# Optimization experiments

Measured on AMD Instinct MI355X. Metric: run time of the kernel, lower is better.

The kernel has to match this reference:

```python
import jax, jax.numpy as jnp
import numpy as np

EPS = 1e-5

def silu(x):
    return x * jax.nn.sigmoid(x)

def layernorm(x, g, b):
    m = jnp.mean(x, axis=-1, keepdims=True)
    v = jnp.var(x, axis=-1, keepdims=True)
    return (x - m) * jax.lax.rsqrt(v + EPS) * g + b

def mamba(x, in_w, conv_w, conv_b, xproj_w, dt_w, dt_b, A_log, Dp, out_w):
    # x: (B, L, d_model)
    B_, L, _ = x.shape
    d_inner, d_conv = conv_w.shape
    d_state = A_log.shape[1]
    dt_rank = dt_w.shape[1]
    xz = x @ in_w.T                     # (B, L, 2*d_inner)
    u, z = jnp.split(xz, 2, axis=-1)
    # causal depthwise conv1d, kernel size d_conv, truncated to L
    up = jnp.pad(u, ((0, 0), (d_conv - 1, 0), (0, 0))).transpose(0, 2, 1)  # (B, C, L+K-1)
    uc = jax.lax.conv_general_dilated(up, conv_w[:, None, :], (1,), 'VALID',
                                      feature_group_count=d_inner)        # (B, C, L)
    u = silu(uc.transpose(0, 2, 1) + conv_b)                               # (B, L, d_inner)
    dbc = u @ xproj_w.T                                                    # (B, L, dt_rank+2*d_state)
    dt, Bm, Cm = jnp.split(dbc, [dt_rank, dt_rank + d_state], axis=-1)
    delta = jax.nn.softplus(dt @ dt_w.T + dt_b)                            # (B, L, d_inner)
    A = -jnp.exp(A_log)                                                    # (d_inner, d_state)
    dA = jnp.exp(delta[..., None] * A)                                     # (B, L, d_inner, d_state)
    dBu = delta[..., None] * Bm[:, :, None, :] * u[..., None]

    def step(h, inp):
        dA_t, dBu_t, C_t = inp
        h = dA_t * h + dBu_t                                               # (B, d_inner, d_state)
        y = jnp.einsum('bdn,bn->bd', h, C_t)
        return h, y

    h0 = jnp.zeros((B_, d_inner, d_state), x.dtype)
    _, ys = jax.lax.scan(step, h0, (dA.transpose(1, 0, 2, 3),
                                    dBu.transpose(1, 0, 2, 3),
                                    Cm.transpose(1, 0, 2)))
    y = ys.transpose(1, 0, 2) + u * Dp
    y = y * silu(z)
    return y @ out_w.T

def decoder_layer(x,
                  f_in_w, f_conv_w, f_conv_b, f_xproj_w, f_dt_w, f_dt_b, f_A_log, f_D, f_out_w,
                  r_in_w, r_conv_w, r_conv_b, r_xproj_w, r_dt_w, r_dt_b, r_A_log, r_D, r_out_w,
                  conv1_w, conv1_b, conv2_w, conv2_b, ln1_g, ln1_b, ln2_g, ln2_b):
    fwd = mamba(x, f_in_w, f_conv_w, f_conv_b, f_xproj_w, f_dt_w, f_dt_b, f_A_log, f_D, f_out_w)
    bwd = jnp.flip(mamba(jnp.flip(x, axis=1), r_in_w, r_conv_w, r_conv_b, r_xproj_w,
                         r_dt_w, r_dt_b, r_A_log, r_D, r_out_w), axis=1)
    x1 = layernorm(x + fwd + bwd, ln1_g, ln1_b)
    # kernel-size-1 Conv1d == pointwise linear; dropout is identity at eval
    y = jax.nn.gelu(x1 @ conv1_w.T + conv1_b, approximate=False)
    y = y @ conv2_w.T + conv2_b
    return layernorm(x1 + y, ln2_g, ln2_b)

def setup_inputs() -> dict:
    key = jax.random.key(0)
    ks = jax.random.split(key, 32)
    d_model, d_state, d_inner, dt_rank, d_ff = 512, 16, 1024, 32, 2048
    B, L = 8, 512
    s = 0.02
    inp = {}
    inp['x'] = jax.random.normal(ks[0], (B, L, d_model), jnp.float32)
    i = 1
    for p in ('f', 'r'):
        inp[p + '_in_w'] = jax.random.normal(ks[i], (2 * d_inner, d_model)) * s; i += 1
        inp[p + '_conv_w'] = jax.random.normal(ks[i], (d_inner, 4)) * 0.2; i += 1
        inp[p + '_conv_b'] = jax.random.normal(ks[i], (d_inner,)) * s; i += 1
        inp[p + '_xproj_w'] = jax.random.normal(ks[i], (dt_rank + 2 * d_state, d_inner)) * s; i += 1
        inp[p + '_dt_w'] = jax.random.normal(ks[i], (d_inner, dt_rank)) * s; i += 1
        inp[p + '_dt_b'] = jax.random.normal(ks[i], (d_inner,)) * s; i += 1
        inp[p + '_A_log'] = jax.random.uniform(ks[i], (d_inner, d_state)); i += 1
        inp[p + '_D'] = jax.random.normal(ks[i], (d_inner,)) * s + 1.0; i += 1
        inp[p + '_out_w'] = jax.random.normal(ks[i], (d_model, d_inner)) * s; i += 1
    inp['conv1_w'] = jax.random.normal(ks[i], (d_ff, d_model)) * s; i += 1
    inp['conv1_b'] = jax.random.normal(ks[i], (d_ff,)) * s; i += 1
    inp['conv2_w'] = jax.random.normal(ks[i], (d_model, d_ff)) * s; i += 1
    inp['conv2_b'] = jax.random.normal(ks[i], (d_model,)) * s; i += 1
    inp['ln1_g'] = jnp.ones((d_model,)); inp['ln1_b'] = jnp.zeros((d_model,))
    inp['ln2_g'] = jnp.ones((d_model,)); inp['ln2_b'] = jnp.zeros((d_model,))
    return inp

def reference(x,
              f_in_w, f_conv_w, f_conv_b, f_xproj_w, f_dt_w, f_dt_b, f_A_log, f_D, f_out_w,
              r_in_w, r_conv_w, r_conv_b, r_xproj_w, r_dt_w, r_dt_b, r_A_log, r_D, r_out_w,
              conv1_w, conv1_b, conv2_w, conv2_b, ln1_g, ln1_b, ln2_g, ln2_b):
    return decoder_layer(x,
                         f_in_w, f_conv_w, f_conv_b, f_xproj_w, f_dt_w, f_dt_b, f_A_log, f_D, f_out_w,
                         r_in_w, r_conv_w, r_conv_b, r_xproj_w, r_dt_w, r_dt_b, r_A_log, r_D, r_out_w,
                         conv1_w, conv1_b, conv2_w, conv2_b, ln1_g, ln1_b, ln2_g, ln2_b)
```

## Files before the change

kernel.cpp:

```cpp
#include <hip/hip_runtime.h>
#include <hip/hip_bf16.h>

#define DEVINL __device__ __forceinline__

typedef short bf16x8 __attribute__((ext_vector_type(8)));
typedef float f32x4 __attribute__((ext_vector_type(4)));
typedef ushort ushort8v __attribute__((ext_vector_type(8)));

static constexpr int Bn = 8, Ln = 512, DM = 512, DI = 1024, DS = 16, DFF = 2048;
static constexpr int Mtok = Bn * Ln;
static constexpr int NCH = 32, CLS = 16;

DEVINL float bf2f(ushort u) { union { uint i; float f; } v; v.i = uint(u) << 16; return v.f; }
DEVINL ushort f2bf(float f) {
  union { float f; uint i; } v; v.f = f;
  uint r = v.i + 0x7FFF + ((v.i >> 16) & 1);
  return ushort(r >> 16);
}

#if __has_builtin(__builtin_amdgcn_exp2f)
#define EXP2F(x) __builtin_amdgcn_exp2f(x)
#else
#define EXP2F(x) __expf((x) * 0.69314718056f)
#endif

#define GLOAD16(gp, lp)                                                        \
  __builtin_amdgcn_global_load_lds(                                            \
      (const __attribute__((address_space(1))) void*)(gp),                     \
      (__attribute__((address_space(3))) void*)(lp), 16, 0, 0)

struct CvtJob { const float* src; ushort* dst; int blk0; int _pad; };
struct CvtTab { CvtJob j[11]; };

__global__ __launch_bounds__(256)
void cvt_k(CvtTab tb, int njobs) {
  const int blk = blockIdx.x;
  int ji = 0;
#pragma unroll
  for (int k = 1; k < 11; ++k)
    if (k < njobs && tb.j[k].blk0 <= blk) ji = k;
  const CvtJob J = tb.j[ji];
  const size_t base = (size_t)(blk - J.blk0) * 2048 + (size_t)threadIdx.x * 8;
  float4 a = *(const float4*)(J.src + base);
  float4 b = *(const float4*)(J.src + base + 4);
  ushort8v o;
  o[0] = f2bf(a.x); o[1] = f2bf(a.y); o[2] = f2bf(a.z); o[3] = f2bf(a.w);
  o[4] = f2bf(b.x); o[5] = f2bf(b.y); o[6] = f2bf(b.z); o[7] = f2bf(b.w);
  *(ushort8v*)(J.dst + base) = o;
}

template<int BM, int BN, int WM, int WN, int EPI, int OUTF32, int DUALK>
__global__ __launch_bounds__(256)
void gemm_lds(const ushort* __restrict__ A0, const ushort* __restrict__ W0,
              void* __restrict__ C0v, const float* __restrict__ bias0,
              const ushort* __restrict__ A1, const ushort* __restrict__ W1,
              void* __restrict__ C1v, const float* __restrict__ bias1,
              const ushort* __restrict__ Ab0, const ushort* __restrict__ Wb0,
              int K, int lda, int ldw, int ldc, int Kb, int ldab, int ldwb)
{
  constexpr int MT = BM / WM / 16, NT = BN / WN / 16;
  constexpr int RA = BM * 32 / 2048, RB = BN * 32 / 2048;
  __shared__ ushort As[BM * 32];
  __shared__ ushort Bs[BN * 32];

  const ushort* Ap = blockIdx.z ? A1 : A0;
  const ushort* Wp = blockIdx.z ? W1 : W0;
  void* Cv         = blockIdx.z ? C1v : C0v;
  const float* bia = blockIdx.z ? bias1 : bias0;

  const int tid = threadIdx.x, lane = tid & 63, wv = tid >> 6;
  const int wm = wv / WN, wn = wv % WN;
  const int mbase = blockIdx.x * BM, nbase = blockIdx.y * BN;
  const int r = lane & 15, ko = (lane >> 4) * 8;

  f32x4 acc[MT][NT];
#pragma unroll
  for (int mi = 0; mi < MT; ++mi)
#pragma unroll
    for (int ni = 0; ni < NT; ++ni) acc[mi][ni] = (f32x4){0.f, 0.f, 0.f, 0.f};

  for (int blkK = 0; blkK < (DUALK ? 2 : 1); ++blkK) {
    const ushort* Au = (DUALK && blkK) ? Ab0 : Ap;
    const ushort* Wu = (DUALK && blkK) ? Wb0 : Wp;
    const int Ku  = (DUALK && blkK) ? Kb : K;
    const int ldau = (DUALK && blkK) ? ldab : lda;
    const int ldwu = (DUALK && blkK) ? ldwb : ldw;

    for (int k0 = 0; k0 < Ku; k0 += 32) {
      __syncthreads();
#pragma unroll
      for (int i = 0; i < RA; ++i) {
        const int e = i * 2048 + wv * 512 + lane * 8;
        const int row = e >> 5, ck = e & 31;
        GLOAD16(Au + (size_t)(mbase + row) * ldau + k0 + ck,
                (ushort*)As + i * 2048 + wv * 512);
      }
#pragma unroll
      for (int i = 0; i < RB; ++i) {
        const int e = i * 2048 + wv * 512 + lane * 8;
        const int row = e >> 5, ck = e & 31;
        GLOAD16(Wu + (size_t)(nbase + row) * ldwu + k0 + ck,
                (ushort*)Bs + i * 2048 + wv * 512);
      }
      __syncthreads();

      bf16x8 af[MT], bfv[NT];
#pragma unroll
      for (int mi = 0; mi < MT; ++mi)
        af[mi] = *(const bf16x8*)&As[(wm * MT * 16 + mi * 16 + r) * 32 + ko];
#pragma unroll
      for (int ni = 0; ni < NT; ++ni)
        bfv[ni] = *(const bf16x8*)&Bs[(wn * NT * 16 + ni * 16 + r) * 32 + ko];
#pragma unroll
      for (int mi = 0; mi < MT; ++mi)
#pragma unroll
        for (int ni = 0; ni < NT; ++ni)
          acc[mi][ni] = __builtin_amdgcn_mfma_f32_16x16x32_bf16(af[mi], bfv[ni], acc[mi][ni], 0, 0, 0);
    }
  }

  const int rr = (lane >> 4) * 4, cc = lane & 15;
#pragma unroll
  for (int ni = 0; ni < NT; ++ni) {
    const int col = nbase + wn * NT * 16 + ni * 16 + cc;
    float bsv = 0.f;
    if (EPI >= 1) bsv = bia[col];
#pragma unroll
    for (int mi = 0; mi < MT; ++mi) {
#pragma unroll
      for (int j = 0; j < 4; ++j) {
        const int row = mbase + wm * MT * 16 + mi * 16 + rr + j;
        float v = acc[mi][ni][j] + bsv;
        if (EPI == 2) v = (v > 20.f) ? v : __logf(1.f + __expf(v));
        if (EPI == 3) v = 0.5f * v * (1.f + erff(v * 0.70710678f));
        if (OUTF32) ((float*)Cv)[(size_t)row * ldc + col] = v;
        else        ((ushort*)Cv)[(size_t)row * ldc + col] = f2bf(v);
      }
    }
  }
}

template<int WAVES_M, int WAVES_N, int MT, int NT, int EPI, int OUTF32, int BLKOUT>
__global__ __launch_bounds__(WAVES_M * WAVES_N * 64)
void gemm_k(const ushort* __restrict__ A0, const ushort* __restrict__ W0,
            void* __restrict__ C0v, const float* __restrict__ bias0,
            const ushort* __restrict__ A1, const ushort* __restrict__ W1,
            void* __restrict__ C1v, const float* __restrict__ bias1,
            int K, int lda, int ldw, int ldc)
{
  const ushort* A   = blockIdx.z ? A1 : A0;
  const ushort* W   = blockIdx.z ? W1 : W0;
  void* Cv          = blockIdx.z ? C1v : C0v;
  const float* bia  = blockIdx.z ? bias1 : bias0;

  const int tid = threadIdx.x, lane = tid & 63, wv = tid >> 6;
  const int wm = wv / WAVES_N, wn = wv % WAVES_N;
  const int r = lane & 15, ko = (lane >> 4) * 8;
  const int mbase = blockIdx.x * (WAVES_M * MT * 16) + wm * (MT * 16);
  const int nbase = blockIdx.y * (WAVES_N * NT * 16) + wn * (NT * 16);

  f32x4 acc[MT][NT];
#pragma unroll
  for (int mi = 0; mi < MT; ++mi)
#pragma unroll
    for (int ni = 0; ni < NT; ++ni) acc[mi][ni] = (f32x4){0.f, 0.f, 0.f, 0.f};

  const ushort* arow[MT];
  const ushort* wrow[NT];
#pragma unroll
  for (int mi = 0; mi < MT; ++mi) arow[mi] = A + (size_t)(mbase + mi * 16 + r) * lda + ko;
#pragma unroll
  for (int ni = 0; ni < NT; ++ni) wrow[ni] = W + (size_t)(nbase + ni * 16 + r) * ldw + ko;
  for (int k0 = 0; k0 < K; k0 += 32) {
    bf16x8 av[MT], bv[NT];
#pragma unroll
    for (int mi = 0; mi < MT; ++mi) av[mi] = *(const bf16x8*)(arow[mi] + k0);
#pragma unroll
    for (int ni = 0; ni < NT; ++ni) bv[ni] = *(const bf16x8*)(wrow[ni] + k0);
#pragma unroll
    for (int mi = 0; mi < MT; ++mi)
#pragma unroll
      for (int ni = 0; ni < NT; ++ni)
        acc[mi][ni] = __builtin_amdgcn_mfma_f32_16x16x32_bf16(av[mi], bv[ni], acc[mi][ni], 0, 0, 0);
  }

  const int rr = (lane >> 4) * 4, cc = lane & 15;
  if constexpr (BLKOUT) {
    __shared__ ushort tile[64][65];
#pragma unroll
    for (int ni = 0; ni < NT; ++ni) {
      const int col = nbase + ni * 16 + cc;
      float bsv = (EPI >= 1) ? bia[col] : 0.f;
#pragma unroll
      for (int mi = 0; mi < MT; ++mi) {
#pragma unroll
        for (int j = 0; j < 4; ++j) {
          float v = acc[mi][ni][j] + bsv;
          if (EPI == 2) v = (v > 20.f) ? v : __logf(1.f + __expf(v));
          const int rl = (wm * MT + mi) * 16 + rr + j;
          const int cl = (wn * NT + ni) * 16 + cc;
          tile[rl][cl] = f2bf(v);
        }
      }
    }
    __syncthreads();
    const int rc = tid >> 6, coll = tid & 63;
    const int mblk = blockIdx.x * (WAVES_M * MT * 16);
    const int nblk = blockIdx.y * (WAVES_N * NT * 16);
    ushort8v o0, o1;
#pragma unroll
    for (int jj = 0; jj < 8; ++jj) {
      o0[jj] = tile[rc * 16 + jj][coll];
      o1[jj] = tile[rc * 16 + 8 + jj][coll];
    }
    const size_t base = ((size_t)((mblk >> 4) + rc) * ldc + nblk + coll) * 16;
    *(ushort8v*)((ushort*)Cv + base) = o0;
    *(ushort8v*)((ushort*)Cv + base + 8) = o1;
  } else {
#pragma unroll
    for (int ni = 0; ni < NT; ++ni) {
      const int col = nbase + ni * 16 + cc;
      float bsv = 0.f;
      if (EPI >= 1) bsv = bia[col];
#pragma unroll
      for (int mi = 0; mi < MT; ++mi) {
#pragma unroll
        for (int j = 0; j < 4; ++j) {
          const int row = mbase + mi * 16 + rr + j;
          float v = acc[mi][ni][j] + bsv;
          if (EPI == 2) v = (v > 20.f) ? v : __logf(1.f + __expf(v));
          if (OUTF32) ((float*)Cv)[(size_t)row * ldc + col] = v;
          else        ((ushort*)Cv)[(size_t)row * ldc + col] = f2bf(v);
        }
      }
    }
  }
}

__global__ __launch_bounds__(256)
void xproj_k(const ushort* __restrict__ A0, const ushort* __restrict__ W0,
             ushort* __restrict__ C0,
             const ushort* __restrict__ A1, const ushort* __restrict__ W1,
             ushort* __restrict__ C1)
{
  const ushort* A = blockIdx.z ? A1 : A0;
  const ushort* W = blockIdx.z ? W1 : W0;
  ushort* C       = blockIdx.z ? C1 : C0;

  const int tid = threadIdx.x, lane = tid & 63, wv = tid >> 6;
  const int r = lane & 15, ko = (lane >> 4) * 8;
  const int mbase = blockIdx.x * 16;
  const int nbase = wv * 16;

  f32x4 acc = (f32x4){0.f, 0.f, 0.f, 0.f};
  const ushort* ap = A + (size_t)(mbase + r) * DI + ko;
  const ushort* wp = W + (size_t)(nbase + r) * DI + ko;
#pragma unroll 4
  for (int k0 = 0; k0 < DI; k0 += 32) {
    const bf16x8 av = *(const bf16x8*)(ap + k0);
    const bf16x8 bv = *(const bf16x8*)(wp + k0);
    acc = __builtin_amdgcn_mfma_f32_16x16x32_bf16(av, bv, acc, 0, 0, 0);
  }
  const int cc = lane & 15, rr = (lane >> 4) * 4;
#pragma unroll
  for (int j = 0; j < 4; ++j)
    C[(size_t)(mbase + rr + j) * 64 + nbase + cc] = f2bf(acc[j]);
}

#define CONV_LOADW(pos, dst)                                                   \
  if ((pos) >= 0 && (pos) < Ln) {                                              \
    const ushort4 xv = *(const ushort4*)(xz + (size_t)(bLn + (pos)) * 2048 + c0); \
    dst[0] = bf2f(xv.x); dst[1] = bf2f(xv.y);                                  \
    dst[2] = bf2f(xv.z); dst[3] = bf2f(xv.w);                                  \
  } else { dst[0] = 0.f; dst[1] = 0.f; dst[2] = 0.f; dst[3] = 0.f; }

#define CONV_STEP(tpos, s)                                                     \
  {                                                                            \
    _Pragma("unroll")                                                          \
    for (int ch = 0; ch < 4; ++ch) {                                           \
      wa[ch] = wb[ch]; wb[ch] = wc[ch]; wc[ch] = wd[ch];                       \
    }                                                                          \
    {                                                                          \
      const ushort4 xv = *(const ushort4*)(xz + (size_t)(bLn + (tpos)) * 2048 + c0); \
      wd[0] = bf2f(xv.x); wd[1] = bf2f(xv.y);                                  \
      wd[2] = bf2f(xv.z); wd[3] = bf2f(xv.w);                                  \
    }                                                                          \
    const ushort4 zv = *(const ushort4*)(xz + (size_t)(bLn + (tpos)) * 2048 + DI + c0); \
    float zf[4];                                                               \
    zf[0] = bf2f(zv.x); zf[1] = bf2f(zv.y); zf[2] = bf2f(zv.z); zf[3] = bf2f(zv.w); \
    ushort4 ur;                                                                \
    _Pragma("unroll")                                                          \
    for (int ch = 0; ch < 4; ++ch) {                                           \
      float sa = bias[ch] + wgt[ch][0] * wa[ch] + wgt[ch][1] * wb[ch]          \
               + wgt[ch][2] * wc[ch] + wgt[ch][3] * wd[ch];                    \
      const ushort su = f2bf(sa / (1.f + __expf(-sa)));                        \
      ubuf[ch][(s) >> 3][(s) & 7] = su;                                        \
      ((ushort*)&ur)[ch] = su;                                                 \
      gbuf[ch][(s) >> 3][(s) & 7] = f2bf(zf[ch] / (1.f + __expf(-zf[ch])));    \
    }                                                                          \
    *(ushort4*)(uo + (size_t)(bLn + (tpos)) * 1024 + c0) = ur;                 \
  }

__global__ __launch_bounds__(256, 2)
void conv_k(const ushort* __restrict__ xz_f, const ushort* __restrict__ xz_r,
            const float* __restrict__ fw, const float* __restrict__ fb,
            const float* __restrict__ rw, const float* __restrict__ rb,
            ushort* __restrict__ u_f, ushort* __restrict__ u_r,
            ushort* __restrict__ ub_f, ushort* __restrict__ ub_r,
            ushort* __restrict__ gb_f, ushort* __restrict__ gb_r)
{
  const int idx = blockIdx.x * 256 + threadIdx.x;
  const int cg = idx & 255, chunk = (idx >> 8) & 31, b = (idx >> 13) & 7, dir = idx >> 16;
  const int c0 = cg * 4;
  const int bLn = b * Ln;

  const ushort* xz = dir ? xz_r : xz_f;
  const float* cw = dir ? rw : fw;
  const float* cb = dir ? rb : fb;
  ushort* uo = dir ? u_r : u_f;
  ushort* ub = dir ? ub_r : ub_f;
  ushort* gb = dir ? gb_r : gb_f;

  float bias[4];
  float wgt[4][4];
#pragma unroll
  for (int ch = 0; ch < 4; ++ch) {
    bias[ch] = cb[c0 + ch];
    const float4 w4 = *(const float4*)(cw + (size_t)(c0 + ch) * 4);
    wgt[ch][0] = w4.x; wgt[ch][1] = w4.y; wgt[ch][2] = w4.z; wgt[ch][3] = w4.w;
  }

  float wa[4], wb[4], wc[4], wd[4];
  ushort8v ubuf[4][2], gbuf[4][2];

  if (!dir) {
    const int t0 = chunk * 16;
    CONV_LOADW(t0 - 3, wb)
    CONV_LOADW(t0 - 2, wc)
    CONV_LOADW(t0 - 1, wd)
#pragma unroll
    for (int s = 0; s < 16; ++s) CONV_STEP(t0 + s, s)
  } else {
    const int t1 = chunk * 16 + 15;
    CONV_LOADW(t1 + 3, wb)
    CONV_LOADW(t1 + 2, wc)
    CONV_LOADW(t1 + 1, wd)
#pragma unroll
    for (int i = 0; i < 16; ++i) CONV_STEP(t1 - i, 15 - i)
  }

  const size_t blkBase = ((size_t)(b * 32 + chunk) * 1024 + c0) * 16;
#pragma unroll
  for (int ch = 0; ch < 4; ++ch) {
    *(ushort8v*)(ub + blkBase + (size_t)ch * 16)     = ubuf[ch][0];
    *(ushort8v*)(ub + blkBase + (size_t)ch * 16 + 8) = ubuf[ch][1];
    *(ushort8v*)(gb + blkBase + (size_t)ch * 16)     = gbuf[ch][0];
    *(ushort8v*)(gb + blkBase + (size_t)ch * 16 + 8) = gbuf[ch][1];
  }
}

#define SCAN1_STEP(s, e)                                                       \
  {                                                                            \
    const float dl = bf2f((ushort)(((e) < 8) ? dv0[(e)] : dv1[(e) - 8]));      \
    const float uv = bf2f((ushort)(((e) < 8) ? uv0[(e)] : uv1[(e) - 8]));      \
    const float du = dl * uv;                                                  \
    S += dl;                                                                   \
    _Pragma("unroll")                                                          \
    for (int g = 0; g < 4; ++g) {                                              \
      const float4 Bv = ((const float4*)Bs[(s)])[g];                           \
      h[g*4+0] = fmaf(EXP2F(dl * a2[g*4+0]), h[g*4+0], du * Bv.x);             \
      h[g*4+1] = fmaf(EXP2F(dl * a2[g*4+1]), h[g*4+1], du * Bv.y);             \
      h[g*4+2] = fmaf(EXP2F(dl * a2[g*4+2]), h[g*4+2], du * Bv.z);             \
      h[g*4+3] = fmaf(EXP2F(dl * a2[g*4+3]), h[g*4+3], du * Bv.w);             \
    }                                                                          \
  }

__global__ __launch_bounds__(256, 4)
void scan1_k(const ushort* __restrict__ db_f, const ushort* __restrict__ db_r,
             const ushort* __restrict__ ub_f, const ushort* __restrict__ ub_r,
             const ushort* __restrict__ dbc_f, const ushort* __restrict__ dbc_r,
             const float* __restrict__ fA, const float* __restrict__ rA,
             float4* __restrict__ hloc, float* __restrict__ Sa)
{
  const int bid = blockIdx.x;
  const int part = bid & 3, chunk = (bid >> 2) & 31, b = (bid >> 7) & 7, dir = bid >> 10;
  const int tid = threadIdx.x, c = part * 256 + tid;
  const int bd = dir * 8 + b;

  const ushort* dblk = dir ? db_r : db_f;
  const ushort* ublk = dir ? ub_r : ub_f;
  const ushort* dbc  = dir ? dbc_r : dbc_f;
  const float*  Alog = dir ? rA : fA;

  __shared__ float Bs[CLS][16];
  {
    const int s = tid >> 4, n = tid & 15;
    const int t = dir ? (Ln - 1 - (chunk * CLS + s)) : (chunk * CLS + s);
    Bs[s][n] = bf2f(dbc[(size_t)(b * Ln + t) * 64 + 32 + n]);
  }
  __syncthreads();

  float a2[16];
  {
    const float4* Ar = (const float4*)(Alog + (size_t)c * 16);
#pragma unroll
    for (int g = 0; g < 4; ++g) {
      float4 av = Ar[g];
      a2[g*4+0] = -__expf(av.x) * 1.44269504f;
      a2[g*4+1] = -__expf(av.y) * 1.44269504f;
      a2[g*4+2] = -__expf(av.z) * 1.44269504f;
      a2[g*4+3] = -__expf(av.w) * 1.44269504f;
    }
  }

  const int sc = dir ? (31 - chunk) : chunk;
  const size_t blkBase = (((size_t)(b * 32 + sc)) * 1024 + c) * 16;
  const ushort8v dv0 = *(const ushort8v*)(dblk + blkBase);
  const ushort8v dv1 = *(const ushort8v*)(dblk + blkBase + 8);
  const ushort8v uv0 = *(const ushort8v*)(ublk + blkBase);
  const ushort8v uv1 = *(const ushort8v*)(ublk + blkBase + 8);

  float h[16];
#pragma unroll
  for (int n = 0; n < 16; ++n) h[n] = 0.f;
  float S = 0.f;

  if (!dir) {
#pragma unroll
    for (int s = 0; s < CLS; ++s) SCAN1_STEP(s, s)
  } else {
#pragma unroll
    for (int s = 0; s < CLS; ++s) SCAN1_STEP(s, 15 - s)
  }

#pragma unroll
  for (int g = 0; g < 4; ++g) {
    const size_t o = ((size_t)g * 16 * NCH + (size_t)bd * NCH + chunk) * 1024 + c;
    hloc[o] = (float4){h[g*4+0], h[g*4+1], h[g*4+2], h[g*4+3]};
  }
  Sa[((size_t)bd * NCH + chunk) * 1024 + c] = S;
}

__global__ __launch_bounds__(256, 4)
void scan2_k(float4* __restrict__ hloc, const float* __restrict__ Sa,
             const float* __restrict__ fA, const float* __restrict__ rA)
{
  const int idx = blockIdx.x * 256 + threadIdx.x;
  const int ng = idx & 3, c = (idx >> 2) & 1023, b = (idx >> 12) & 7, dir = idx >> 15;
  const int bd = dir * 8 + b;
  const float* Alog = dir ? rA : fA;
  float a2[4];
  {
    const float4 av = *(const float4*)(Alog + (size_t)c * 16 + ng * 4);
    a2[0] = -__expf(av.x) * 1.44269504f;
    a2[1] = -__expf(av.y) * 1.44269504f;
    a2[2] = -__expf(av.z) * 1.44269504f;
    a2[3] = -__expf(av.w) * 1.44269504f;
  }
  float4 h = (float4){0.f, 0.f, 0.f, 0.f};
#pragma unroll
  for (int k = 0; k < NCH; ++k) {
    const size_t o = ((size_t)ng * 16 * NCH + (size_t)bd * NCH + k) * 1024 + c;
    const float S = Sa[((size_t)bd * NCH + k) * 1024 + c];
    const float4 hl = hloc[o];
    hloc[o] = h;
    h.x = fmaf(EXP2F(a2[0] * S), h.x, hl.x);
    h.y = fmaf(EXP2F(a2[1] * S), h.y, hl.y);
    h.z = fmaf(EXP2F(a2[2] * S), h.z, hl.z);
    h.w = fmaf(EXP2F(a2[3] * S), h.w, hl.w);
  }
}

#define SCAN3_STEP(s, e)                                                       \
  {                                                                            \
    const float dl = bf2f((ushort)(((e) < 8) ? dv0[(e)] : dv1[(e) - 8]));      \
    const float uv = bf2f((ushort)(((e) < 8) ? uv0[(e)] : uv1[(e) - 8]));      \
    const float gg = bf2f((ushort)(((e) < 8) ? gv0[(e)] : gv1[(e) - 8]));      \
    const float du = dl * uv;                                                  \
    float y = 0.f;                                                             \
    _Pragma("unroll")                                                          \
    for (int g = 0; g < 4; ++g) {                                              \
      const float4 Bv = ((const float4*)Bs[(s)])[g];                           \
      const float4 Cw = ((const float4*)Cs[(s)])[g];                           \
      h[g*4+0] = fmaf(EXP2F(dl * a2[g*4+0]), h[g*4+0], du * Bv.x);             \
      y = fmaf(h[g*4+0], Cw.x, y);                                             \
      h[g*4+1] = fmaf(EXP2F(dl * a2[g*4+1]), h[g*4+1], du * Bv.y);             \
      y = fmaf(h[g*4+1], Cw.y, y);                                             \
      h[g*4+2] = fmaf(EXP2F(dl * a2[g*4+2]), h[g*4+2], du * Bv.z);             \
      y = fmaf(h[g*4+2], Cw.z, y);                                             \
      h[g*4+3] = fmaf(EXP2F(dl * a2[g*4+3]), h[g*4+3], du * Bv.w);             \
      y = fmaf(h[g*4+3], Cw.w, y);                                             \
    }                                                                          \
    *ymp = f2bf((y + uv * Dc) * gg);                                           \
    ymp += stp;                                                                \
  }

__global__ __launch_bounds__(256, 4)
void scan3_k(const ushort* __restrict__ db_f, const ushort* __restrict__ db_r,
             const ushort* __restrict__ ub_f, const ushort* __restrict__ ub_r,
             const ushort* __restrict__ dbc_f, const ushort* __restrict__ dbc_r,
             const ushort* __restrict__ gb_f, const ushort* __restrict__ gb_r,
             const float* __restrict__ fA, const float* __restrict__ fD,
             const float* __restrict__ rA, const float* __restrict__ rD,
             const float4* __restrict__ hin,
             ushort* __restrict__ ym_f, ushort* __restrict__ ym_r)
{
  const int bid = blockIdx.x;
  const int part = bid & 3, chunk = (bid >> 2) & 31, b = (bid >> 7) & 7, dir = bid >> 10;
  const int tid = threadIdx.x, c = part * 256 + tid;
  const int bd = dir * 8 + b;

  const ushort* dblk = dir ? db_r : db_f;
  const ushort* ublk = dir ? ub_r : ub_f;
  const ushort* gblk = dir ? gb_r : gb_f;
  const ushort* dbc  = dir ? dbc_r : dbc_f;
  const float*  Alog = dir ? rA : fA;
  const float*  Dw   = dir ? rD : fD;
  ushort* ym         = dir ? ym_r : ym_f;

  __shared__ float Bs[CLS][16], Cs[CLS][16];
  {
    const int s = tid >> 5, k = tid & 31;
#pragma unroll
    for (int p = 0; p < 2; ++p) {
      const int ss = s + p * 8;
      const int t = dir ? (Ln - 1 - (chunk * CLS + ss)) : (chunk * CLS + ss);
      const float val = bf2f(dbc[(size_t)(b * Ln + t) * 64 + 32 + k]);
      if (k < 16) Bs[ss][k] = val; else Cs[ss][k - 16] = val;
    }
  }
  __syncthreads();

  float a2[16];
  {
    const float4* Ar = (const float4*)(Alog + (size_t)c * 16);
#pragma unroll
    for (int g = 0; g < 4; ++g) {
      float4 av = Ar[g];
      a2[g*4+0] = -__expf(av.x) * 1.44269504f;
      a2[g*4+1] = -__expf(av.y) * 1.44269504f;
      a2[g*4+2] = -__expf(av.z) * 1.44269504f;
      a2[g*4+3] = -__expf(av.w) * 1.44269504f;
    }
  }
  const float Dc = Dw[c];

  const int sc = dir ? (31 - chunk) : chunk;
  const size_t blkBase = (((size_t)(b * 32 + sc)) * 1024 + c) * 16;
  const ushort8v dv0 = *(const ushort8v*)(dblk + blkBase);
  const ushort8v dv1 = *(const ushort8v*)(dblk + blkBase + 8);
  const ushort8v uv0 = *(const ushort8v*)(ublk + blkBase);
  const ushort8v uv1 = *(const ushort8v*)(ublk + blkBase + 8);
  const ushort8v gv0 = *(const ushort8v*)(gblk + blkBase);
  const ushort8v gv1 = *(const ushort8v*)(gblk + blkBase + 8);

  float h[16];
#pragma unroll
  for (int g = 0; g < 4; ++g) {
    const size_t o = ((size_t)g * 16 * NCH + (size_t)bd * NCH + chunk) * 1024 + c;
    const float4 hv = hin[o];
    h[g*4+0] = hv.x; h[g*4+1] = hv.y; h[g*4+2] = hv.z; h[g*4+3] = hv.w;
  }

  const int t0 = dir ? (Ln - 1 - chunk * CLS) : (chunk * CLS);
  const int stp = (dir ? -1 : 1) * DI;
  ushort* ymp = ym + (size_t)(b * Ln + t0) * DI + c;

  if (!dir) {
#pragma unroll
    for (int s = 0; s < CLS; ++s) SCAN3_STEP(s, s)
  } else {
#pragma unroll
    for (int s = 0; s < CLS; ++s) SCAN3_STEP(s, 15 - s)
  }
}

template<int OUTF32>
__global__ __launch_bounds__(256)
void ln_k(const ushort* __restrict__ a, const ushort* __restrict__ b,
          const float* __restrict__ g, const float* __restrict__ bb,
          void* __restrict__ outv)
{
  const int row = blockIdx.x, tid = threadIdx.x;
  const size_t base = (size_t)row * DM;
  float v0 = bf2f(a[base + tid]) + bf2f(b[base + tid]);
  float v1 = bf2f(a[base + tid + 256]) + bf2f(b[base + tid + 256]);
  float s1 = v0 + v1, s2 = v0 * v0 + v1 * v1;
  for (int o = 32; o; o >>= 1) { s1 += __shfl_down(s1, o); s2 += __shfl_down(s2, o); }
  __shared__ float l1[4], l2[4];
  const int wv = tid >> 6, ln = tid & 63;
  if (ln == 0) { l1[wv] = s1; l2[wv] = s2; }
  __syncthreads();
  const float t1 = l1[0] + l1[1] + l1[2] + l1[3];
  const float t2 = l2[0] + l2[1] + l2[2] + l2[3];
  const float mean = t1 * (1.f / 512.f);
  const float var = t2 * (1.f / 512.f) - mean * mean;
  const float rs = rsqrtf(var + 1e-5f);
  const float o0 = (v0 - mean) * rs * g[tid] + bb[tid];
  const float o1 = (v1 - mean) * rs * g[tid + 256] + bb[tid + 256];
  if (OUTF32) {
    ((float*)outv)[base + tid] = o0;
    ((float*)outv)[base + tid + 256] = o1;
  } else {
    ((ushort*)outv)[base + tid] = f2bf(o0);
    ((ushort*)outv)[base + tid + 256] = f2bf(o1);
  }
}

extern "C" void kernel_launch(void* const* d_in, const int* in_sizes, int n_in,
                              void* d_out, int out_size, void* d_ws, size_t ws_size,
                              hipStream_t stream)
{
  const float* x        = (const float*)d_in[0];
  const float* f_in_w   = (const float*)d_in[1];
  const float* f_conv_w = (const float*)d_in[2];
  const float* f_conv_b = (const float*)d_in[3];
  const float* f_xproj  = (const float*)d_in[4];
  const float* f_dt_w   = (const float*)d_in[5];
  const float* f_dt_b   = (const float*)d_in[6];
  const float* f_A_log  = (const float*)d_in[7];
  const float* f_D      = (const float*)d_in[8];
  const float* f_out_w  = (const float*)d_in[9];
  const float* r_in_w   = (const float*)d_in[10];
  const float* r_conv_w = (const float*)d_in[11];
  const float* r_conv_b = (const float*)d_in[12];
  const float* r_xproj  = (const float*)d_in[13];
  const float* r_dt_w   = (const float*)d_in[14];
  const float* r_dt_b   = (const float*)d_in[15];
  const float* r_A_log  = (const float*)d_in[16];
  const float* r_D      = (const float*)d_in[17];
  const float* r_out_w  = (const float*)d_in[18];
  const float* conv1_w  = (const float*)d_in[19];
  const float* conv1_b  = (const float*)d_in[20];
  const float* conv2_w  = (const float*)d_in[21];
  const float* conv2_b  = (const float*)d_in[22];
  const float* ln1_g    = (const float*)d_in[23];
  const float* ln1_b    = (const float*)d_in[24];
  const float* ln2_g    = (const float*)d_in[25];
  const float* ln2_b    = (const float*)d_in[26];

  char* ws = (char*)d_ws;
  size_t off = 0;
  auto alloc = [&](size_t bytes) -> void* {
    void* p = ws + off;
    off += (bytes + 255) & ~(size_t)255;
    return p;
  };
  ushort* x_b     = (ushort*)alloc((size_t)Mtok * DM * 2);
  ushort* f_inw_b = (ushort*)alloc((size_t)2 * DI * DM * 2);
  ushort* r_inw_b = (ushort*)alloc((size_t)2 * DI * DM * 2);
  ushort* f_xp_b  = (ushort*)alloc((size_t)64 * DI * 2);
  ushort* r_xp_b  = (ushort*)alloc((size_t)64 * DI * 2);
  ushort* f_dtw_b = (ushort*)alloc((size_t)DI * 32 * 2);
  ushort* r_dtw_b = (ushort*)alloc((size_t)DI * 32 * 2);
  ushort* f_ow_b  = (ushort*)alloc((size_t)DM * DI * 2);
  ushort* r_ow_b  = (ushort*)alloc((size_t)DM * DI * 2);
  ushort* c1w_b   = (ushort*)alloc((size_t)DFF * DM * 2);
  ushort* c2w_b   = (ushort*)alloc((size_t)DM * DFF * 2);
  ushort* xz_f    = (ushort*)alloc((size_t)Mtok * 2048 * 2);
  ushort* xz_r    = (ushort*)alloc((size_t)Mtok * 2048 * 2);
  ushort* u_f     = (ushort*)alloc((size_t)Mtok * DI * 2);
  ushort* u_r     = (ushort*)alloc((size_t)Mtok * DI * 2);
  ushort* ub_f    = (ushort*)alloc((size_t)Mtok * DI * 2);
  ushort* ub_r    = (ushort*)alloc((size_t)Mtok * DI * 2);
  ushort* gb_f    = (ushort*)alloc((size_t)Mtok * DI * 2);
  ushort* gb_r    = (ushort*)alloc((size_t)Mtok * DI * 2);
  ushort* dbc_f   = (ushort*)alloc((size_t)Mtok * 64 * 2);
  ushort* dbc_r   = (ushort*)alloc((size_t)Mtok * 64 * 2);
  ushort* db_f    = (ushort*)alloc((size_t)Mtok * DI * 2);
  ushort* db_r    = (ushort*)alloc((size_t)Mtok * DI * 2);
  ushort* ym_f    = (ushort*)alloc((size_t)Mtok * DI * 2);
  ushort* ym_r    = (ushort*)alloc((size_t)Mtok * DI * 2);
  ushort* mo      = (ushort*)alloc((size_t)Mtok * DM * 2);
  ushort* x1      = (ushort*)alloc((size_t)Mtok * DM * 2);
  ushort* h1b     = (ushort*)alloc((size_t)Mtok * DFF * 2);
  ushort* y2      = (ushort*)alloc((size_t)Mtok * DM * 2);
  float4* hloc    = (float4*)alloc((size_t)4 * 16 * NCH * 1024 * 16);
  float*  Sa      = (float*)alloc((size_t)16 * NCH * 1024 * 4);
  (void)ws_size; (void)in_sizes; (void)n_in; (void)out_size;

  {
    CvtTab tb;
    int blk = 0, ji = 0;
    auto add = [&](const float* s, ushort* d, int n) {
      tb.j[ji].src = s; tb.j[ji].dst = d; tb.j[ji].blk0 = blk; tb.j[ji]._pad = 0;
      blk += n / 2048; ++ji;
    };
    add(x,       x_b,     Mtok * DM);
    add(f_in_w,  f_inw_b, 2 * DI * DM);
    add(r_in_w,  r_inw_b, 2 * DI * DM);
    add(f_xproj, f_xp_b,  64 * DI);
    add(r_xproj, r_xp_b,  64 * DI);
    add(f_dt_w,  f_dtw_b, DI * 32);
    add(r_dt_w,  r_dtw_b, DI * 32);
    add(f_out_w, f_ow_b,  DM * DI);
    add(r_out_w, r_ow_b,  DM * DI);
    add(conv1_w, c1w_b,   DFF * DM);
    add(conv2_w, c2w_b,   DM * DFF);
    cvt_k<<<dim3(blk), 256, 0, stream>>>(tb, ji);
  }

  gemm_lds<128, 128, 2, 2, 0, 0, 0><<<dim3(32, 16, 2), 256, 0, stream>>>(
      x_b, f_inw_b, xz_f, nullptr, x_b, r_inw_b, xz_r, nullptr,
      nullptr, nullptr, DM, DM, DM, 2048, 0, 0, 0);

  conv_k<<<dim3(512), 256, 0, stream>>>(
      xz_f, xz_r, f_conv_w, f_conv_b, r_conv_w, r_conv_b,
      u_f, u_r, ub_f, ub_r, gb_f, gb_r);

  xproj_k<<<dim3(256, 1, 2), 256, 0, stream>>>(
      u_f, f_xp_b, dbc_f, u_r, r_xp_b, dbc_r);

  gemm_k<4, 1, 1, 4, 2, 0, 1><<<dim3(64, 16, 2), 256, 0, stream>>>(
      dbc_f, f_dtw_b, db_f, f_dt_b, dbc_r, r_dtw_b, db_r, r_dt_b,
      32, 64, 32, DI);

  scan1_k<<<dim3(2048), 256, 0, stream>>>(
      db_f, db_r, ub_f, ub_r, dbc_f, dbc_r, f_A_log, r_A_log, hloc, Sa);
  scan2_k<<<dim3(256), 256, 0, stream>>>(hloc, Sa, f_A_log, r_A_log);
  scan3_k<<<dim3(2048), 256, 0, stream>>>(
      db_f, db_r, ub_f, ub_r, dbc_f, dbc_r, gb_f, gb_r,
      f_A_log, f_D, r_A_log, r_D, hloc, ym_f, ym_r);

  gemm_lds<64, 64, 2, 2, 0, 0, 1><<<dim3(64, 8, 1), 256, 0, stream>>>(
      ym_f, f_ow_b, mo, nullptr, nullptr, nullptr, nullptr, nullptr,
      ym_r, r_ow_b, DI, DI, DI, DM, DI, DI, DI);

  ln_k<0><<<dim3(Mtok), 256, 0, stream>>>(x_b, mo, ln1_g, ln1_b, x1);

  gemm_lds<128, 128, 2, 2, 3, 0, 0><<<dim3(32, 16, 1), 256, 0, stream>>>(
      x1, c1w_b, h1b, conv1_b, nullptr, nullptr, nullptr, nullptr,
      nullptr, nullptr, DM, DM, DM, DFF, 0, 0, 0);

  gemm_lds<64, 64, 2, 2, 1, 0, 0><<<dim3(64, 8, 1), 256, 0, stream>>>(
      h1b, c2w_b, y2, conv2_b, nullptr, nullptr, nullptr, nullptr,
      nullptr, nullptr, DFF, DFF, DFF, DM, 0, 0, 0);

  ln_k<1><<<dim3(Mtok), 256, 0, stream>>>(x1, y2, ln2_g, ln2_b, (float*)d_out);
}
```

Baseline: 240.8 us.

## Fuse dt projection and softplus into xproj kernel; use tanh-form GELU

The separate dt-projection GEMM launch is removed. Each xproj block now writes its 16x32 dt slice to LDS, then runs the dt_w MFMA plus bias and softplus, storing delta in the blocked layout scan expects. This saves a kernel launch and a global round trip of the dt columns. The FFN GELU epilogue also swaps erf for a tanh approximation computed with exp2, which is cheaper but slightly changes numerics.

```diff
diff --git a/kernel.cpp b/kernel.cpp
--- a/kernel.cpp
+++ b/kernel.cpp
@@ -131,8 +131,10 @@
       for (int j = 0; j < 4; ++j) {
         const int row = mbase + wm * MT * 16 + mi * 16 + rr + j;
         float v = acc[mi][ni][j] + bsv;
-        if (EPI == 2) v = (v > 20.f) ? v : __logf(1.f + __expf(v));
-        if (EPI == 3) v = 0.5f * v * (1.f + erff(v * 0.70710678f));
+        if (EPI == 3) {
+          const float t = v * (0.7978845608f + v * v * 0.0356774081f);
+          v = v / (1.f + EXP2F(t * -2.885390082f));
+        }
         if (OUTF32) ((float*)Cv)[(size_t)row * ldc + col] = v;
         else        ((ushort*)Cv)[(size_t)row * ldc + col] = f2bf(v);
       }
@@ -140,112 +142,23 @@
   }
 }
 
-template<int WAVES_M, int WAVES_N, int MT, int NT, int EPI, int OUTF32, int BLKOUT>
-__global__ __launch_bounds__(WAVES_M * WAVES_N * 64)
-void gemm_k(const ushort* __restrict__ A0, const ushort* __restrict__ W0,
-            void* __restrict__ C0v, const float* __restrict__ bias0,
-            const ushort* __restrict__ A1, const ushort* __restrict__ W1,
-            void* __restrict__ C1v, const float* __restrict__ bias1,
-            int K, int lda, int ldw, int ldc)
-{
-  const ushort* A   = blockIdx.z ? A1 : A0;
-  const ushort* W   = blockIdx.z ? W1 : W0;
-  void* Cv          = blockIdx.z ? C1v : C0v;
-  const float* bia  = blockIdx.z ? bias1 : bias0;
-
-  const int tid = threadIdx.x, lane = tid & 63, wv = tid >> 6;
-  const int wm = wv / WAVES_N, wn = wv % WAVES_N;
-  const int r = lane & 15, ko = (lane >> 4) * 8;
-  const int mbase = blockIdx.x * (WAVES_M * MT * 16) + wm * (MT * 16);
-  const int nbase = blockIdx.y * (WAVES_N * NT * 16) + wn * (NT * 16);
-
-  f32x4 acc[MT][NT];
-#pragma unroll
-  for (int mi = 0; mi < MT; ++mi)
-#pragma unroll
-    for (int ni = 0; ni < NT; ++ni) acc[mi][ni] = (f32x4){0.f, 0.f, 0.f, 0.f};
-
-  const ushort* arow[MT];
-  const ushort* wrow[NT];
-#pragma unroll
-  for (int mi = 0; mi < MT; ++mi) arow[mi] = A + (size_t)(mbase + mi * 16 + r) * lda + ko;
-#pragma unroll
-  for (int ni = 0; ni < NT; ++ni) wrow[ni] = W + (size_t)(nbase + ni * 16 + r) * ldw + ko;
-  for (int k0 = 0; k0 < K; k0 += 32) {
-    bf16x8 av[MT], bv[NT];
-#pragma unroll
-    for (int mi = 0; mi < MT; ++mi) av[mi] = *(const bf16x8*)(arow[mi] + k0);
-#pragma unroll
-    for (int ni = 0; ni < NT; ++ni) bv[ni] = *(const bf16x8*)(wrow[ni] + k0);
-#pragma unroll
-    for (int mi = 0; mi < MT; ++mi)
-#pragma unroll
-      for (int ni = 0; ni < NT; ++ni)
-        acc[mi][ni] = __builtin_amdgcn_mfma_f32_16x16x32_bf16(av[mi], bv[ni], acc[mi][ni], 0, 0, 0);
-  }
-
-  const int rr = (lane >> 4) * 4, cc = lane & 15;
-  if constexpr (BLKOUT) {
-    __shared__ ushort tile[64][65];
-#pragma unroll
-    for (int ni = 0; ni < NT; ++ni) {
-      const int col = nbase + ni * 16 + cc;
-      float bsv = (EPI >= 1) ? bia[col] : 0.f;
-#pragma unroll
-      for (int mi = 0; mi < MT; ++mi) {
-#pragma unroll
-        for (int j = 0; j < 4; ++j) {
-          float v = acc[mi][ni][j] + bsv;
-          if (EPI == 2) v = (v > 20.f) ? v : __logf(1.f + __expf(v));
-          const int rl = (wm * MT + mi) * 16 + rr + j;
-          const int cl = (wn * NT + ni) * 16 + cc;
-          tile[rl][cl] = f2bf(v);
-        }
-      }
-    }
-    __syncthreads();
-    const int rc = tid >> 6, coll = tid & 63;
-    const int mblk = blockIdx.x * (WAVES_M * MT * 16);
-    const int nblk = blockIdx.y * (WAVES_N * NT * 16);
-    ushort8v o0, o1;
-#pragma unroll
-    for (int jj = 0; jj < 8; ++jj) {
-      o0[jj] = tile[rc * 16 + jj][coll];
-      o1[jj] = tile[rc * 16 + 8 + jj][coll];
-    }
-    const size_t base = ((size_t)((mblk >> 4) + rc) * ldc + nblk + coll) * 16;
-    *(ushort8v*)((ushort*)Cv + base) = o0;
-    *(ushort8v*)((ushort*)Cv + base + 8) = o1;
-  } else {
-#pragma unroll
-    for (int ni = 0; ni < NT; ++ni) {
-      const int col = nbase + ni * 16 + cc;
-      float bsv = 0.f;
-      if (EPI >= 1) bsv = bia[col];
-#pragma unroll
-      for (int mi = 0; mi < MT; ++mi) {
-#pragma unroll
-        for (int j = 0; j < 4; ++j) {
-          const int row = mbase + mi * 16 + rr + j;
-          float v = acc[mi][ni][j] + bsv;
-          if (EPI == 2) v = (v > 20.f) ? v : __logf(1.f + __expf(v));
-          if (OUTF32) ((float*)Cv)[(size_t)row * ldc + col] = v;
-          else        ((ushort*)Cv)[(size_t)row * ldc + col] = f2bf(v);
-        }
-      }
-    }
-  }
-}
-
 __global__ __launch_bounds__(256)
 void xproj_k(const ushort* __restrict__ A0, const ushort* __restrict__ W0,
              ushort* __restrict__ C0,
              const ushort* __restrict__ A1, const ushort* __restrict__ W1,
-             ushort* __restrict__ C1)
-{
-  const ushort* A = blockIdx.z ? A1 : A0;
-  const ushort* W = blockIdx.z ? W1 : W0;
-  ushort* C       = blockIdx.z ? C1 : C0;
+             ushort* __restrict__ C1,
+             const ushort* __restrict__ dtw0, const float* __restrict__ dtb0,
+             const ushort* __restrict__ dtw1, const float* __restrict__ dtb1,
+             ushort* __restrict__ db0, ushort* __restrict__ db1)
+{
+  const ushort* A   = blockIdx.z ? A1 : A0;
+  const ushort* W   = blockIdx.z ? W1 : W0;
+  ushort* C         = blockIdx.z ? C1 : C0;
+  const ushort* dtw = blockIdx.z ? dtw1 : dtw0;
+  const float*  dtb = blockIdx.z ? dtb1 : dtb0;
+  ushort* db        = blockIdx.z ? db1 : db0;
+
+  __shared__ ushort dt_lds[16][32];
 
   const int tid = threadIdx.x, lane = tid & 63, wv = tid >> 6;
   const int r = lane & 15, ko = (lane >> 4) * 8;
@@ -262,9 +175,35 @@
     acc = __builtin_amdgcn_mfma_f32_16x16x32_bf16(av, bv, acc, 0, 0, 0);
   }
   const int cc = lane & 15, rr = (lane >> 4) * 4;
-#pragma unroll
-  for (int j = 0; j < 4; ++j)
-    C[(size_t)(mbase + rr + j) * 64 + nbase + cc] = f2bf(acc[j]);
+  if (nbase < 32) {
+#pragma unroll
+    for (int j = 0; j < 4; ++j)
+      dt_lds[rr + j][nbase + cc] = f2bf(acc[j]);
+  } else {
+#pragma unroll
+    for (int j = 0; j < 4; ++j)
+      C[(size_t)(mbase + rr + j) * 64 + nbase + cc] = f2bf(acc[j]);
+  }
+  __syncthreads();
+
+  const bf16x8 ad = *(const bf16x8*)&dt_lds[r][ko];
+  const int cwbase = wv * 256;
+#pragma unroll
+  for (int ni = 0; ni < 16; ++ni) {
+    const bf16x8 bvv = *(const bf16x8*)(dtw + (size_t)(cwbase + ni * 16 + r) * 32 + ko);
+    f32x4 accd = (f32x4){0.f, 0.f, 0.f, 0.f};
+    accd = __builtin_amdgcn_mfma_f32_16x16x32_bf16(ad, bvv, accd, 0, 0, 0);
+    const int col = cwbase + ni * 16 + cc;
+    const float bsv = dtb[col];
+    ushort4 ov;
+#pragma unroll
+    for (int j = 0; j < 4; ++j) {
+      float v = accd[j] + bsv;
+      v = (v > 20.f) ? v : __logf(1.f + __expf(v));
+      ((ushort*)&ov)[j] = f2bf(v);
+    }
+    *(ushort4*)(db + ((size_t)blockIdx.x * 1024 + col) * 16 + rr) = ov;
+  }
 }
 
 #define CONV_LOADW(pos, dst)                                                   \
@@ -709,11 +648,8 @@
       u_f, u_r, ub_f, ub_r, gb_f, gb_r);
 
   xproj_k<<<dim3(256, 1, 2), 256, 0, stream>>>(
-      u_f, f_xp_b, dbc_f, u_r, r_xp_b, dbc_r);
-
-  gemm_k<4, 1, 1, 4, 2, 0, 1><<<dim3(64, 16, 2), 256, 0, stream>>>(
-      dbc_f, f_dtw_b, db_f, f_dt_b, dbc_r, r_dtw_b, db_r, r_dt_b,
-      32, 64, 32, DI);
+      u_f, f_xp_b, dbc_f, u_r, r_xp_b, dbc_r,
+      f_dtw_b, f_dt_b, r_dtw_b, r_dt_b, db_f, db_r);
 
   scan1_k<<<dim3(2048), 256, 0, stream>>>(
       db_f, db_r, ub_f, ub_r, dbc_f, dbc_r, f_A_log, r_A_log, hloc, Sa);
```

Result: no change. 238.8 us (-0.8%).
